# Optimization experiments

Measured on AMD Instinct MI355X. Metric: run time of the kernel, lower is better.

The kernel has to match this reference:

```python
import jax, jax.numpy as jnp
import numpy as np

B, C, H, W = 8, 256, 64, 64
EPS = 1e-5


def _mk_conv_bn(key, oc, ic):
    k = jax.random.split(key, 6)
    return dict(
        w=jax.random.normal(k[0], (oc, ic), jnp.float32) * 0.01,  # trunc-normal approx, stddev 0.01
        b=jnp.zeros((oc,), jnp.float32),
        s=jax.random.uniform(k[1], (oc,), jnp.float32, 0.5, 1.5),   # BN scale
        t=jax.random.normal(k[2], (oc,), jnp.float32) * 0.1,        # BN shift
        m=jax.random.normal(k[3], (oc,), jnp.float32) * 0.1,        # BN running mean
        v=jax.random.uniform(k[4], (oc,), jnp.float32, 0.5, 1.5),   # BN running var
    )


def setup_inputs() -> dict:
    key = jax.random.key(0)
    ks = jax.random.split(key, 6)
    d = {"x": jax.random.normal(ks[0], (B, C, H, W), jnp.float32)}
    for i, (oc, ic) in zip([1, 2, 3, 4], [(C // 8, C), (C // 8, C), (C // 2, C), (C, C // 2)]):
        p = _mk_conv_bn(ks[i], oc, ic)
        for name, val in p.items():
            d[f"{name}{i}"] = val
    d["gamma"] = jnp.asarray(0.5, jnp.float32)
    return d


def _cbn(x, w, b, s, t, m, v, relu=True):
    # conv1x1 + BatchNorm(eval) [+ ReLU]; dropout is identity at inference
    y = jnp.einsum('bchw,oc->bohw', x, w) + b[None, :, None, None]
    scale = (s / jnp.sqrt(v + EPS))[None, :, None, None]
    y = (y - m[None, :, None, None]) * scale + t[None, :, None, None]
    return jax.nn.relu(y) if relu else y


def _maxpool2(x):
    b, c, h, w = x.shape
    return x.reshape(b, c, h // 2, 2, w // 2, 2).max(axis=(3, 5))


def reference(x, w1, b1, s1, t1, m1, v1, w2, b2, s2, t2, m2, v2,
              w3, b3, s3, t3, m3, v3, w4, b4, s4, t4, m4, v4, gamma):
    b, c, h, w = x.shape
    f = _maxpool2(_cbn(x, w1, b1, s1, t1, m1, v1))   # (B, C/8, H/2, W/2)
    g = _cbn(x, w2, b2, s2, t2, m2, v2)              # (B, C/8, H, W)
    hh = _maxpool2(_cbn(x, w3, b3, s3, t3, m3, v3))  # (B, C/2, H/2, W/2)
    hw, hw4 = h * w, (h // 2) * (w // 2)
    f = f.reshape(b, c // 8, hw4).transpose(0, 2, 1)  # (B, HW/4, C/8)
    g = g.reshape(b, c // 8, hw)                      # (B, C/8, HW)
    s = jnp.einsum('bnk,bkm->bnm', f, g)              # (B, HW/4, HW)
    beta = jax.nn.softmax(s, axis=1)                  # softmax over dim=1, as in source
    hh = hh.reshape(b, c // 2, hw4)                   # (B, C/2, HW/4)
    o = jnp.einsum('bcn,bnm->bcm', hh, beta).reshape(b, c // 2, h, w)
    out = _cbn(o, w4, b4, s4, t4, m4, v4, relu=False)
    return gamma * out + x
```

## Files before the change

kernel.cpp:

```cpp
#include <hip/hip_runtime.h>
#include <hip/hip_bf16.h>

#define HW   4096
#define HW4  1024
#define EPS  1e-5f
#define SM_SHIFT 20.0f

typedef __attribute__((ext_vector_type(8)))  short    bf16x8;
typedef __attribute__((ext_vector_type(4)))  float    f32x4;

__device__ __forceinline__ short f2bs(float f) {
    union { float f; unsigned u; } v; v.f = f;
    unsigned r = v.u + 0x7FFFu + ((v.u >> 16) & 1u);
    return (short)(r >> 16);
}
__device__ __forceinline__ int swz64(int r, int c)  { return (r << 6) + ((c ^ (r & 7))  << 3); }
__device__ __forceinline__ int swz128(int r, int c) { return (r << 7) + ((c ^ (r & 15)) << 3); }
__device__ __forceinline__ int p40(int r, int c)    { return r * 40 + c * 8; }

__global__ __launch_bounds__(512) void conv123pool(
    const float* __restrict__ x,
    const float* __restrict__ w1, const float* __restrict__ b1, const float* __restrict__ s1,
    const float* __restrict__ t1, const float* __restrict__ m1, const float* __restrict__ v1,
    const float* __restrict__ w2, const float* __restrict__ b2, const float* __restrict__ s2,
    const float* __restrict__ t2, const float* __restrict__ m2, const float* __restrict__ v2,
    const float* __restrict__ w3, const float* __restrict__ b3, const float* __restrict__ s3,
    const float* __restrict__ t3, const float* __restrict__ m3, const float* __restrict__ v3,
    const float* __restrict__ w4,
    short* __restrict__ w4T,
    short* __restrict__ gbufT, short* __restrict__ fbufT, short* __restrict__ hhbuf)
{
    __shared__ __align__(16) short Wl[192 * 64];
    __shared__ __align__(16) short Xl[128 * 64];
    __shared__ float alB[192], beB[192];

    const int t = threadIdx.x;
    const int lane = t & 63, wv = t >> 6;
    const int quad = lane >> 4, l16 = lane & 15;
    const int ptile = blockIdx.x;
    const int bz    = blockIdx.y;
    const int pBase = ptile * 128;
    const int wcol  = (wv & 1) * 32;
    const int woch  = (wv >> 1) * 48;

    const int xp2 = (t & 63) * 2, xkg = t >> 6;
    const float* xBase = x + ((size_t)bz * 256 + xkg * 8) * HW + pBase + xp2;

    float2 fvA[8], fvB[8];
    #pragma unroll
    for (int j = 0; j < 8; ++j) fvA[j] = *(const float2*)(xBase + (size_t)j * HW);

    if (bz == 0) {
        int idx = (ptile * 512 + t) * 2;
        float2 a = *(const float2*)(w4 + idx);
        short2 o; o.x = f2bs(a.x); o.y = f2bs(a.y);
        *(short2*)&w4T[idx] = o;
    }

    if (t < 192) {
        int j = t;
        float pb, ps, ptv, pm, pv;
        if (j < 32)      { pb = b1[j]; ps = s1[j]; ptv = t1[j]; pm = m1[j]; pv = v1[j]; }
        else if (j < 64) { int c = j - 32; pb = b2[c]; ps = s2[c]; ptv = t2[c]; pm = m2[c]; pv = v2[c]; }
        else             { int c = j - 64; pb = b3[c]; ps = s3[c]; ptv = t3[c]; pm = m3[c]; pv = v3[c]; }
        float al = ps * rsqrtf(pv + EPS);
        alB[t] = al; beB[t] = (pb - pm) * al + ptv;
    }

    const f32x4 fzero = {0.f, 0.f, 0.f, 0.f};
    f32x4 acc[3][4];
    #pragma unroll
    for (int i = 0; i < 3; ++i)
        #pragma unroll
        for (int j = 0; j < 4; ++j) acc[i][j] = fzero;

    const int ptOff0 = wcol, ptOff1 = wcol + 16, ptOff2 = wcol + 64, ptOff3 = wcol + 80;

#define K1_CHUNK(KC, CUR, NXT)                                                        \
    {                                                                                 \
        _Pragma("unroll")                                                             \
        for (int i = 0; i < 2; ++i) {                                                 \
            int idx = t + i * 512;                                                    \
            if (i == 0 || t < 256) {                                                  \
                int oc = idx >> 2, kb = (idx & 3) * 16;                               \
                const float* wp = (oc < 32) ? (w1 + oc * 256)                         \
                                : (oc < 64) ? (w2 + (oc - 32) * 256)                  \
                                            : (w3 + (oc - 64) * 256);                 \
                wp += (KC) * 64 + kb;                                                 \
                float4 a = *(const float4*)(wp);                                      \
                float4 b = *(const float4*)(wp + 4);                                  \
                float4 c = *(const float4*)(wp + 8);                                  \
                float4 d = *(const float4*)(wp + 12);                                 \
                bf16x8 lo, hi;                                                        \
                lo[0]=f2bs(a.x); lo[1]=f2bs(a.y); lo[2]=f2bs(a.z); lo[3]=f2bs(a.w);   \
                lo[4]=f2bs(b.x); lo[5]=f2bs(b.y); lo[6]=f2bs(b.z); lo[7]=f2bs(b.w);   \
                hi[0]=f2bs(c.x); hi[1]=f2bs(c.y); hi[2]=f2bs(c.z); hi[3]=f2bs(c.w);   \
                hi[4]=f2bs(d.x); hi[5]=f2bs(d.y); hi[6]=f2bs(d.z); hi[7]=f2bs(d.w);   \
                *(bf16x8*)&Wl[swz64(oc, (kb >> 3))]     = lo;                         \
                *(bf16x8*)&Wl[swz64(oc, (kb >> 3) + 1)] = hi;                         \
            }                                                                         \
        }                                                                             \
        if ((KC) < 3) {                                                               \
            const float* xn = xBase + (size_t)(((KC) + 1) * 64) * HW;                 \
            _Pragma("unroll")                                                         \
            for (int j2 = 0; j2 < 8; ++j2) NXT[j2] = *(const float2*)(xn + (size_t)j2 * HW); \
        }                                                                             \
        {                                                                             \
            bf16x8 va, vb;                                                            \
            _Pragma("unroll")                                                         \
            for (int j2 = 0; j2 < 8; ++j2) { va[j2] = f2bs(CUR[j2].x); vb[j2] = f2bs(CUR[j2].y); } \
            *(bf16x8*)&Xl[swz64(xp2,     xkg)] = va;                                  \
            *(bf16x8*)&Xl[swz64(xp2 + 1, xkg)] = vb;                                  \
        }                                                                             \
        __syncthreads();                                                              \
        _Pragma("unroll")                                                             \
        for (int kk = 0; kk < 2; ++kk) {                                              \
            bf16x8 bfr[4];                                                            \
            bfr[0] = *(const bf16x8*)&Xl[swz64(ptOff0 + l16, kk * 4 + quad)];         \
            bfr[1] = *(const bf16x8*)&Xl[swz64(ptOff1 + l16, kk * 4 + quad)];         \
            bfr[2] = *(const bf16x8*)&Xl[swz64(ptOff2 + l16, kk * 4 + quad)];         \
            bfr[3] = *(const bf16x8*)&Xl[swz64(ptOff3 + l16, kk * 4 + quad)];         \
            _Pragma("unroll")                                                         \
            for (int tt = 0; tt < 3; ++tt) {                                          \
                bf16x8 afr = *(const bf16x8*)&Wl[swz64(woch + tt*16 + l16, kk*4 + quad)]; \
                _Pragma("unroll")                                                     \
                for (int pt = 0; pt < 4; ++pt)                                        \
                    acc[tt][pt] = __builtin_amdgcn_mfma_f32_16x16x32_bf16(afr, bfr[pt], acc[tt][pt], 0, 0, 0); \
            }                                                                         \
        }                                                                             \
        __syncthreads();                                                              \
    }

    K1_CHUNK(0, fvA, fvB)
    K1_CHUNK(1, fvB, fvA)
    K1_CHUNK(2, fvA, fvB)
    K1_CHUNK(3, fvB, fvA)
#undef K1_CHUNK

    #pragma unroll
    for (int tt = 0; tt < 3; ++tt) {
        #pragma unroll
        for (int r = 0; r < 4; ++r) {
            int j = woch + tt * 16 + quad * 4 + r;
            float al = alB[j], be = beB[j];
            float y[4];
            y[0] = fmaxf(acc[tt][0][r] * al + be, 0.f);
            y[1] = fmaxf(acc[tt][1][r] * al + be, 0.f);
            y[2] = fmaxf(acc[tt][2][r] * al + be, 0.f);
            y[3] = fmaxf(acc[tt][3][r] * al + be, 0.f);
            if (j >= 32 && j < 64) {
                size_t mb = (size_t)bz * 4096 + pBase;
                int kk = j - 32;
                gbufT[(mb + ptOff0 + l16) * 32 + kk] = f2bs(y[0]);
                gbufT[(mb + ptOff1 + l16) * 32 + kk] = f2bs(y[1]);
                gbufT[(mb + ptOff2 + l16) * 32 + kk] = f2bs(y[2]);
                gbufT[(mb + ptOff3 + l16) * 32 + kk] = f2bs(y[3]);
            } else {
                #pragma unroll
                for (int c = 0; c < 2; ++c) {
                    float v  = fmaxf(y[c], y[c + 2]);
                    float po = fmaxf(v, __shfl_xor(v, 1));
                    if ((l16 & 1) == 0) {
                        int col = wcol + c * 16 + l16;
                        int n = ptile * 32 + (col >> 1);
                        if (j < 32) fbufT[((size_t)bz * 1024 + n) * 32 + j] = f2bs(po);
                        else        hhbuf[((size_t)bz * 128 + (j - 64)) * HW4 + n] = f2bs(po);
                    }
                }
            }
        }
    }
}

__global__ __launch_bounds__(256, 2) void attn_conv4(
    const short* __restrict__ gbufT,
    const short* __restrict__ fbufT,
    const short* __restrict__ hhbuf,
    const float* __restrict__ x,
    const short* __restrict__ w4T, const float* __restrict__ b4, const float* __restrict__ s4,
    const float* __restrict__ t4, const float* __restrict__ m4, const float* __restrict__ v4,
    const float* __restrict__ gamma, float* __restrict__ out)
{
    __shared__ __align__(16) short smem[24576];
    __shared__ float alB4[256], beB4[256];
    __shared__ float Zl[64];
    short* sT0  = smem;
    short* sT1  = smem + 4096;
    short* hhl0 = smem + 8192;
    short* hhl1 = smem + 16384;
    short* o_l  = smem;
    short* Wl4  = smem + 8192;

    const int t = threadIdx.x;
    const int lane = t & 63, wv = t >> 6;
    const int quad = lane >> 4, l16 = lane & 15;
    const int bz = blockIdx.y;
    const int m0 = blockIdx.x * 64;
    const f32x4 fzero = {0.f, 0.f, 0.f, 0.f};

    {
        float al = s4[t] * rsqrtf(v4[t] + EPS);
        alB4[t] = al; beB4[t] = (b4[t] - m4[t]) * al + t4[t];
    }

    const short* fT = fbufT + (size_t)bz * 1024 * 32;
    const short* hB = hhbuf + (size_t)bz * 128 * HW4;
    const int hrow = t >> 3, hnc = t & 7;

    bf16x8 bg = *(const bf16x8*)&gbufT[((size_t)bz * 4096 + m0 + wv * 16 + l16) * 32 + quad * 8];

    bf16x8 fr[4], hr[4];
    #pragma unroll
    for (int nt = 0; nt < 4; ++nt)
        fr[nt] = *(const bf16x8*)&fT[(nt * 16 + l16) * 32 + quad * 8];
    #pragma unroll
    for (int i = 0; i < 4; ++i)
        hr[i] = *(const bf16x8*)(hB + (size_t)(i * 32 + hrow) * HW4 + hnc * 8);

    float psum = 0.f;
    f32x4 oacc[2][4];
    #pragma unroll
    for (int a = 0; a < 2; ++a)
        #pragma unroll
        for (int b = 0; b < 4; ++b) oacc[a][b] = fzero;

    #pragma unroll 2
    for (int it = 0; it < 16; ++it) {
        const int n0n = ((it + 1) & 15) << 6;
        short* hb = (it & 1) ? hhl1 : hhl0;
        short* sT = (it & 1) ? sT1  : sT0;

        #pragma unroll
        for (int i = 0; i < 4; ++i)
            *(bf16x8*)&hb[swz64(i * 32 + hrow, hnc)] = hr[i];
        #pragma unroll
        for (int i = 0; i < 4; ++i)
            hr[i] = *(const bf16x8*)(hB + (size_t)(i * 32 + hrow) * HW4 + n0n + hnc * 8);

        f32x4 sacc[4];
        #pragma unroll
        for (int nt = 0; nt < 4; ++nt)
            sacc[nt] = __builtin_amdgcn_mfma_f32_16x16x32_bf16(fr[nt], bg, fzero, 0, 0, 0);
        #pragma unroll
        for (int nt = 0; nt < 4; ++nt)
            fr[nt] = *(const bf16x8*)&fT[(n0n + nt * 16 + l16) * 32 + quad * 8];

        #pragma unroll
        for (int nt = 0; nt < 4; ++nt) {
            short4 ev;
            #pragma unroll
            for (int r = 0; r < 4; ++r) {
                float e = __expf(sacc[nt][r] - SM_SHIFT);
                psum += e;
                ((short*)&ev)[r] = f2bs(e);
            }
            *(short4*)&sT[swz64(wv * 16 + l16, nt * 2 + (quad >> 1)) + (quad & 1) * 4] = ev;
        }

        __syncthreads();

        #pragma unroll
        for (int kk = 0; kk < 2; ++kk) {
            bf16x8 ah0 = *(const bf16x8*)&hb[swz64(wv * 32 + l16,      kk * 4 + quad)];
            bf16x8 ah1 = *(const bf16x8*)&hb[swz64(wv * 32 + 16 + l16, kk * 4 + quad)];
            bf16x8 bs[4];
            #pragma unroll
            for (int mt = 0; mt < 4; ++mt)
                bs[mt] = *(const bf16x8*)&sT[swz64(mt * 16 + l16, kk * 4 + quad)];
            #pragma unroll
            for (int mt = 0; mt < 4; ++mt) {
                oacc[0][mt] = __builtin_amdgcn_mfma_f32_16x16x32_bf16(ah0, bs[mt], oacc[0][mt], 0, 0, 0);
                oacc[1][mt] = __builtin_amdgcn_mfma_f32_16x16x32_bf16(ah1, bs[mt], oacc[1][mt], 0, 0, 0);
            }
        }
    }

    psum += __shfl_xor(psum, 16);
    psum += __shfl_xor(psum, 32);
    if (quad == 0) Zl[wv * 16 + l16] = psum;
    __syncthreads();

    #pragma unroll
    for (int mt = 0; mt < 4; ++mt) {
        float iv = 1.0f / Zl[mt * 16 + l16];
        #pragma unroll
        for (int ct2 = 0; ct2 < 2; ++ct2) {
            short4 ov;
            #pragma unroll
            for (int r = 0; r < 4; ++r) ((short*)&ov)[r] = f2bs(oacc[ct2][mt][r] * iv);
            *(short4*)&o_l[swz128(mt * 16 + l16, wv * 4 + ct2 * 2 + (quad >> 1)) + (quad & 1) * 4] = ov;
        }
    }

    f32x4 acc4[4][4];
    #pragma unroll
    for (int i = 0; i < 4; ++i)
        #pragma unroll
        for (int j = 0; j < 4; ++j) acc4[i][j] = fzero;

    const int wrow = t >> 2, wcid = t & 3;
    bf16x8 Wr[4];
    #pragma unroll
    for (int g = 0; g < 4; ++g)
        Wr[g] = *(const bf16x8*)(w4T + (g * 64 + wrow) * 128 + wcid * 8);

    #pragma unroll
    for (int k0i = 0; k0i < 4; ++k0i) {
        const int k0 = k0i * 32;
        __syncthreads();
        #pragma unroll
        for (int g = 0; g < 4; ++g)
            *(bf16x8*)&Wl4[p40(g * 64 + wrow, wcid)] = Wr[g];
        if (k0i < 3) {
            #pragma unroll
            for (int g = 0; g < 4; ++g)
                Wr[g] = *(const bf16x8*)(w4T + (g * 64 + wrow) * 128 + k0 + 32 + wcid * 8);
        }
        __syncthreads();
        bf16x8 bfr[4];
        #pragma unroll
        for (int mt = 0; mt < 4; ++mt)
            bfr[mt] = *(const bf16x8*)&o_l[swz128(mt * 16 + l16, (k0 >> 3) + quad)];
        #pragma unroll
        for (int ot = 0; ot < 4; ++ot) {
            bf16x8 afr = *(const bf16x8*)&Wl4[p40(wv * 64 + ot * 16 + l16, quad)];
            #pragma unroll
            for (int mt = 0; mt < 4; ++mt)
                acc4[ot][mt] = __builtin_amdgcn_mfma_f32_16x16x32_bf16(afr, bfr[mt], acc4[ot][mt], 0, 0, 0);
        }
    }

    float gm = gamma[0];
    #pragma unroll
    for (int ot = 0; ot < 4; ++ot) {
        #pragma unroll
        for (int r = 0; r < 4; ++r) {
            int oc = wv * 64 + ot * 16 + quad * 4 + r;
            float al = alB4[oc], be = beB4[oc];
            #pragma unroll
            for (int mt = 0; mt < 4; ++mt) {
                int p = m0 + mt * 16 + l16;
                float y  = acc4[ot][mt][r] * al + be;
                float xo = x[((size_t)bz * 256 + oc) * HW + p];
                out[((size_t)bz * 256 + oc) * HW + p] = gm * y + xo;
            }
        }
    }
}

extern "C" void kernel_launch(void* const* d_in, const int* in_sizes, int n_in,
                              void* d_out, int out_size, void* d_ws, size_t ws_size,
                              hipStream_t stream)
{
    const float* x  = (const float*)d_in[0];
    const float* w1 = (const float*)d_in[1];
    const float* b1 = (const float*)d_in[2];
    const float* s1 = (const float*)d_in[3];
    const float* t1 = (const float*)d_in[4];
    const float* m1 = (const float*)d_in[5];
    const float* v1 = (const float*)d_in[6];
    const float* w2 = (const float*)d_in[7];
    const float* b2 = (const float*)d_in[8];
    const float* s2 = (const float*)d_in[9];
    const float* t2 = (const float*)d_in[10];
    const float* m2 = (const float*)d_in[11];
    const float* v2 = (const float*)d_in[12];
    const float* w3 = (const float*)d_in[13];
    const float* b3 = (const float*)d_in[14];
    const float* s3 = (const float*)d_in[15];
    const float* t3 = (const float*)d_in[16];
    const float* m3 = (const float*)d_in[17];
    const float* v3 = (const float*)d_in[18];
    const float* w4 = (const float*)d_in[19];
    const float* b4 = (const float*)d_in[20];
    const float* s4 = (const float*)d_in[21];
    const float* t4 = (const float*)d_in[22];
    const float* m4 = (const float*)d_in[23];
    const float* v4 = (const float*)d_in[24];
    const float* gm = (const float*)d_in[25];
    float* out = (float*)d_out;

    short* gbufT = (short*)d_ws;
    short* fbufT = gbufT + (size_t)8 * 4096 * 32;
    short* hhbuf = fbufT + (size_t)8 * 1024 * 32;
    short* w4T   = hhbuf + (size_t)8 * 128 * 1024;

    conv123pool<<<dim3(32, 8), 512, 0, stream>>>(
        x, w1, b1, s1, t1, m1, v1, w2, b2, s2, t2, m2, v2, w3, b3, s3, t3, m3, v3,
        w4, w4T, gbufT, fbufT, hhbuf);
    attn_conv4<<<dim3(64, 8), 256, 0, stream>>>(
        gbufT, fbufT, hhbuf, x, w4T, b4, s4, t4, m4, v4, gm, out);
}
```

Measured before the change: 158.5 us.

## Preload conv weights to LDS, double-buffer X tiles, use lgkm-only barriers

The conv123pool kernel now converts all four K-chunks of the w1/w2/w3 weights to bf16 once, up front, into a larger LDS buffer. It also double-buffers the X tile so each chunk needs one barrier instead of two, and the next chunk's global loads overlap the current MFMAs. The remaining __syncthreads in the attention/output kernel are replaced with a barrier that only waits on LDS counters, so outstanding global prefetches are not drained at each barrier. The trade-off is a much larger LDS footprint in the conv kernel, which can reduce occupancy, and a longer serial weight-conversion prologue.

```diff
diff --git a/kernel.cpp b/kernel.cpp
--- a/kernel.cpp
+++ b/kernel.cpp
@@ -17,6 +17,12 @@
 __device__ __forceinline__ int swz64(int r, int c)  { return (r << 6) + ((c ^ (r & 7))  << 3); }
 __device__ __forceinline__ int swz128(int r, int c) { return (r << 7) + ((c ^ (r & 15)) << 3); }
 __device__ __forceinline__ int p40(int r, int c)    { return r * 40 + c * 8; }
+
+__device__ __forceinline__ void bar_lgk() {
+    asm volatile("s_waitcnt lgkmcnt(0)" ::: "memory");
+    __builtin_amdgcn_s_barrier();
+    __builtin_amdgcn_sched_barrier(0);
+}
 
 __global__ __launch_bounds__(512) void conv123pool(
     const float* __restrict__ x,
@@ -30,8 +36,8 @@
     short* __restrict__ w4T,
     short* __restrict__ gbufT, short* __restrict__ fbufT, short* __restrict__ hhbuf)
 {
-    __shared__ __align__(16) short Wl[192 * 64];
-    __shared__ __align__(16) short Xl[128 * 64];
+    __shared__ __align__(16) short Wl[4 * 192 * 64];
+    __shared__ __align__(16) short Xl[2 * 128 * 64];
     __shared__ float alB[192], beB[192];
 
     const int t = threadIdx.x;
@@ -67,6 +73,32 @@
         alB[t] = al; beB[t] = (pb - pm) * al + ptv;
     }
 
+    #pragma unroll
+    for (int kc = 0; kc < 4; ++kc) {
+        #pragma unroll
+        for (int i = 0; i < 2; ++i) {
+            int idx = t + i * 512;
+            if (i == 0 || t < 256) {
+                int oc = idx >> 2, kb = (idx & 3) * 16;
+                const float* wp = (oc < 32) ? (w1 + oc * 256)
+                                : (oc < 64) ? (w2 + (oc - 32) * 256)
+                                            : (w3 + (oc - 64) * 256);
+                wp += kc * 64 + kb;
+                float4 a = *(const float4*)(wp);
+                float4 b = *(const float4*)(wp + 4);
+                float4 c = *(const float4*)(wp + 8);
+                float4 d = *(const float4*)(wp + 12);
+                bf16x8 lo, hi;
+                lo[0]=f2bs(a.x); lo[1]=f2bs(a.y); lo[2]=f2bs(a.z); lo[3]=f2bs(a.w);
+                lo[4]=f2bs(b.x); lo[5]=f2bs(b.y); lo[6]=f2bs(b.z); lo[7]=f2bs(b.w);
+                hi[0]=f2bs(c.x); hi[1]=f2bs(c.y); hi[2]=f2bs(c.z); hi[3]=f2bs(c.w);
+                hi[4]=f2bs(d.x); hi[5]=f2bs(d.y); hi[6]=f2bs(d.z); hi[7]=f2bs(d.w);
+                *(bf16x8*)&Wl[kc * 12288 + swz64(oc, (kb >> 3))]     = lo;
+                *(bf16x8*)&Wl[kc * 12288 + swz64(oc, (kb >> 3) + 1)] = hi;
+            }
+        }
+    }
+
     const f32x4 fzero = {0.f, 0.f, 0.f, 0.f};
     f32x4 acc[3][4];
     #pragma unroll
@@ -76,66 +108,43 @@
 
     const int ptOff0 = wcol, ptOff1 = wcol + 16, ptOff2 = wcol + 64, ptOff3 = wcol + 80;
 
-#define K1_CHUNK(KC, CUR, NXT)                                                        \
-    {                                                                                 \
+#define K1_COMMIT(XB, CUR)                                                            \
+    {   bf16x8 va, vb;                                                                \
         _Pragma("unroll")                                                             \
-        for (int i = 0; i < 2; ++i) {                                                 \
-            int idx = t + i * 512;                                                    \
-            if (i == 0 || t < 256) {                                                  \
-                int oc = idx >> 2, kb = (idx & 3) * 16;                               \
-                const float* wp = (oc < 32) ? (w1 + oc * 256)                         \
-                                : (oc < 64) ? (w2 + (oc - 32) * 256)                  \
-                                            : (w3 + (oc - 64) * 256);                 \
-                wp += (KC) * 64 + kb;                                                 \
-                float4 a = *(const float4*)(wp);                                      \
-                float4 b = *(const float4*)(wp + 4);                                  \
-                float4 c = *(const float4*)(wp + 8);                                  \
-                float4 d = *(const float4*)(wp + 12);                                 \
-                bf16x8 lo, hi;                                                        \
-                lo[0]=f2bs(a.x); lo[1]=f2bs(a.y); lo[2]=f2bs(a.z); lo[3]=f2bs(a.w);   \
-                lo[4]=f2bs(b.x); lo[5]=f2bs(b.y); lo[6]=f2bs(b.z); lo[7]=f2bs(b.w);   \
-                hi[0]=f2bs(c.x); hi[1]=f2bs(c.y); hi[2]=f2bs(c.z); hi[3]=f2bs(c.w);   \
-                hi[4]=f2bs(d.x); hi[5]=f2bs(d.y); hi[6]=f2bs(d.z); hi[7]=f2bs(d.w);   \
-                *(bf16x8*)&Wl[swz64(oc, (kb >> 3))]     = lo;                         \
-                *(bf16x8*)&Wl[swz64(oc, (kb >> 3) + 1)] = hi;                         \
-            }                                                                         \
+        for (int j2 = 0; j2 < 8; ++j2) { va[j2] = f2bs(CUR[j2].x); vb[j2] = f2bs(CUR[j2].y); } \
+        *(bf16x8*)&Xl[(XB) * 8192 + swz64(xp2,     xkg)] = va;                        \
+        *(bf16x8*)&Xl[(XB) * 8192 + swz64(xp2 + 1, xkg)] = vb;                        \
+    }
+#define K1_PREF(KC, NXT)                                                              \
+    {   const float* xn = xBase + (size_t)((KC) * 64) * HW;                           \
+        _Pragma("unroll")                                                             \
+        for (int j2 = 0; j2 < 8; ++j2) NXT[j2] = *(const float2*)(xn + (size_t)j2 * HW); \
+    }
+#define K1_MFMA(XB, KC)                                                               \
+    _Pragma("unroll")                                                                 \
+    for (int kk = 0; kk < 2; ++kk) {                                                  \
+        bf16x8 bfr[4];                                                                \
+        bfr[0] = *(const bf16x8*)&Xl[(XB) * 8192 + swz64(ptOff0 + l16, kk * 4 + quad)]; \
+        bfr[1] = *(const bf16x8*)&Xl[(XB) * 8192 + swz64(ptOff1 + l16, kk * 4 + quad)]; \
+        bfr[2] = *(const bf16x8*)&Xl[(XB) * 8192 + swz64(ptOff2 + l16, kk * 4 + quad)]; \
+        bfr[3] = *(const bf16x8*)&Xl[(XB) * 8192 + swz64(ptOff3 + l16, kk * 4 + quad)]; \
+        _Pragma("unroll")                                                             \
+        for (int tt = 0; tt < 3; ++tt) {                                              \
+            bf16x8 afr = *(const bf16x8*)&Wl[(KC) * 12288 + swz64(woch + tt*16 + l16, kk*4 + quad)]; \
+            _Pragma("unroll")                                                         \
+            for (int pt = 0; pt < 4; ++pt)                                            \
+                acc[tt][pt] = __builtin_amdgcn_mfma_f32_16x16x32_bf16(afr, bfr[pt], acc[tt][pt], 0, 0, 0); \
         }                                                                             \
-        if ((KC) < 3) {                                                               \
-            const float* xn = xBase + (size_t)(((KC) + 1) * 64) * HW;                 \
-            _Pragma("unroll")                                                         \
-            for (int j2 = 0; j2 < 8; ++j2) NXT[j2] = *(const float2*)(xn + (size_t)j2 * HW); \
-        }                                                                             \
-        {                                                                             \
-            bf16x8 va, vb;                                                            \
-            _Pragma("unroll")                                                         \
-            for (int j2 = 0; j2 < 8; ++j2) { va[j2] = f2bs(CUR[j2].x); vb[j2] = f2bs(CUR[j2].y); } \
-            *(bf16x8*)&Xl[swz64(xp2,     xkg)] = va;                                  \
-            *(bf16x8*)&Xl[swz64(xp2 + 1, xkg)] = vb;                                  \
-        }                                                                             \
-        __syncthreads();                                                              \
-        _Pragma("unroll")                                                             \
-        for (int kk = 0; kk < 2; ++kk) {                                              \
-            bf16x8 bfr[4];                                                            \
-            bfr[0] = *(const bf16x8*)&Xl[swz64(ptOff0 + l16, kk * 4 + quad)];         \
-            bfr[1] = *(const bf16x8*)&Xl[swz64(ptOff1 + l16, kk * 4 + quad)];         \
-            bfr[2] = *(const bf16x8*)&Xl[swz64(ptOff2 + l16, kk * 4 + quad)];         \
-            bfr[3] = *(const bf16x8*)&Xl[swz64(ptOff3 + l16, kk * 4 + quad)];         \
-            _Pragma("unroll")                                                         \
-            for (int tt = 0; tt < 3; ++tt) {                                          \
-                bf16x8 afr = *(const bf16x8*)&Wl[swz64(woch + tt*16 + l16, kk*4 + quad)]; \
-                _Pragma("unroll")                                                     \
-                for (int pt = 0; pt < 4; ++pt)                                        \
-                    acc[tt][pt] = __builtin_amdgcn_mfma_f32_16x16x32_bf16(afr, bfr[pt], acc[tt][pt], 0, 0, 0); \
-            }                                                                         \
-        }                                                                             \
-        __syncthreads();                                                              \
-    }
-
-    K1_CHUNK(0, fvA, fvB)
-    K1_CHUNK(1, fvB, fvA)
-    K1_CHUNK(2, fvA, fvB)
-    K1_CHUNK(3, fvB, fvA)
-#undef K1_CHUNK
+    }
+
+    K1_COMMIT(0, fvA)  K1_PREF(1, fvB)  bar_lgk();  K1_MFMA(0, 0)
+    K1_COMMIT(1, fvB)  K1_PREF(2, fvA)  bar_lgk();  K1_MFMA(1, 1)
+    K1_COMMIT(0, fvA)  K1_PREF(3, fvB)  bar_lgk();  K1_MFMA(0, 2)
+    K1_COMMIT(1, fvB)                   bar_lgk();  K1_MFMA(1, 3)
+
+#undef K1_COMMIT
+#undef K1_PREF
+#undef K1_MFMA
 
     #pragma unroll
     for (int tt = 0; tt < 3; ++tt) {
@@ -257,7 +266,7 @@
             *(short4*)&sT[swz64(wv * 16 + l16, nt * 2 + (quad >> 1)) + (quad & 1) * 4] = ev;
         }
 
-        __syncthreads();
+        bar_lgk();
 
         #pragma unroll
         for (int kk = 0; kk < 2; ++kk) {
@@ -278,7 +287,7 @@
     psum += __shfl_xor(psum, 16);
     psum += __shfl_xor(psum, 32);
     if (quad == 0) Zl[wv * 16 + l16] = psum;
-    __syncthreads();
+    bar_lgk();
 
     #pragma unroll
     for (int mt = 0; mt < 4; ++mt) {
@@ -307,7 +316,7 @@
     #pragma unroll
     for (int k0i = 0; k0i < 4; ++k0i) {
         const int k0 = k0i * 32;
-        __syncthreads();
+        bar_lgk();
         #pragma unroll
         for (int g = 0; g < 4; ++g)
             *(bf16x8*)&Wl4[p40(g * 64 + wrow, wcid)] = Wr[g];
@@ -316,7 +325,7 @@
             for (int g = 0; g < 4; ++g)
                 Wr[g] = *(const bf16x8*)(w4T + (g * 64 + wrow) * 128 + k0 + 32 + wcid * 8);
         }
-        __syncthreads();
+        bar_lgk();
         bf16x8 bfr[4];
         #pragma unroll
         for (int mt = 0; mt < 4; ++mt)
```

Result: slower. 162.0 us (+2.2%).
